# Kernel optimization log

Hardware: AMD Instinct MI355X
Metric: run time of the kernel (lower is better)

## Reference

```python
import jax, jax.numpy as jnp
import numpy as np

B, S = 16, 512
VOCAB = 32000
EMB = 512
HID = 1024
LAT = 256
NLAYERS = 2


def rnn_layer(x_seq, h0, w_ih, w_hh, b_ih, b_hh):
    # x_seq: [B, S, in_dim], h0: [B, H]; vanilla tanh RNN (nn.RNN semantics)
    # precompute input projection outside the scan
    xw = jnp.einsum('bsi,hi->bsh', x_seq, w_ih) + b_ih + b_hh  # [B, S, H]

    def step(h, xt):
        h_new = jnp.tanh(xt + h @ w_hh.T)
        return h_new, h_new

    _, ys = jax.lax.scan(step, h0, jnp.swapaxes(xw, 0, 1))  # scan over time
    return jnp.swapaxes(ys, 0, 1)  # [B, S, H]


def setup_inputs() -> dict:
    key = jax.random.key(0)
    ks = jax.random.split(key, 16)
    sc = 0.02
    inp = {
        'z': jax.random.normal(ks[0], (B, LAT), dtype=jnp.float32),
        'inp': jax.random.randint(ks[1], (B, S), 0, VOCAB),
        'emb_table': jax.random.normal(ks[2], (VOCAB, EMB), dtype=jnp.float32) * sc,
        'l2h_w': jax.random.normal(ks[3], (LAT, HID * NLAYERS), dtype=jnp.float32) * sc,
        'l2h_b': jnp.zeros((HID * NLAYERS,), dtype=jnp.float32),
        'w_ih0': jax.random.normal(ks[4], (HID, EMB), dtype=jnp.float32) * sc,
        'w_hh0': jax.random.normal(ks[5], (HID, HID), dtype=jnp.float32) * sc,
        'b_ih0': jnp.zeros((HID,), dtype=jnp.float32),
        'b_hh0': jnp.zeros((HID,), dtype=jnp.float32),
        'w_ih1': jax.random.normal(ks[6], (HID, HID), dtype=jnp.float32) * sc,
        'w_hh1': jax.random.normal(ks[7], (HID, HID), dtype=jnp.float32) * sc,
        'b_ih1': jnp.zeros((HID,), dtype=jnp.float32),
        'b_hh1': jnp.zeros((HID,), dtype=jnp.float32),
        'pred_w': jax.random.normal(ks[8], (HID, VOCAB), dtype=jnp.float32) * sc,
        'pred_b': jnp.zeros((VOCAB,), dtype=jnp.float32),
    }
    return inp


def reference(z, inp, emb_table, l2h_w, l2h_b, w_ih0, w_hh0, b_ih0, b_hh0,
              w_ih1, w_hh1, b_ih1, b_hh1, pred_w, pred_b):
    batch = z.shape[0]
    # latent2hidden, then view(hidden_factor, batch, H) as in torch (flat reshape)
    hidden = z @ l2h_w + l2h_b                      # [B, H*L]
    hidden = hidden.reshape(NLAYERS, batch, HID)     # [L, B, H]
    x = emb_table[inp]                               # [B, S, EMB]
    h1 = rnn_layer(x, hidden[0], w_ih0, w_hh0, b_ih0, b_hh0)   # [B, S, H]
    h2 = rnn_layer(h1, hidden[1], w_ih1, w_hh1, b_ih1, b_hh1)  # [B, S, H]
    logits = h2 @ pred_w + pred_b                    # [B, S, VOCAB]
    return logits
```

## Files before the change

kernel.cpp:

```cpp
#include <hip/hip_runtime.h>
#include <hip/hip_bf16.h>

#define BB 16
#define SS 512
#define VOCAB 32000
#define EMB 512
#define HID 1024
#define LAT 256

typedef __attribute__((ext_vector_type(8))) short bf16x8v;
typedef __attribute__((ext_vector_type(4))) float f32x4v;

__device__ __forceinline__ unsigned short f2b(float f) {
  unsigned int u = __float_as_uint(f);
  unsigned int r = (u + 0x7fffu + ((u >> 16) & 1u)) >> 16;
  return (unsigned short)r;
}

__device__ __forceinline__ float b2f(unsigned short s) {
  return __uint_as_float(((unsigned int)s) << 16);
}

__device__ __forceinline__ float fast_tanh(float x) {
  float t = fminf(fmaxf(x * 2.8853900817779268f, -60.f), 60.f);
  float e = __builtin_amdgcn_exp2f(t);
  return (e - 1.f) * __builtin_amdgcn_rcpf(e + 1.f);
}

__device__ __forceinline__ bf16x8v load16_coherent(const unsigned short* p) {
  bf16x8v r;
  asm volatile("global_load_dwordx4 %0, %1, off sc0 sc1"
               : "=v"(r) : "v"(p) : "memory");
  return r;
}

#define WAITV(n)                                                   \
  do {                                                             \
    asm volatile("s_waitcnt vmcnt(" #n ")" ::: "memory");          \
    __builtin_amdgcn_sched_barrier(0);                             \
  } while (0)

#define MCHUNK(HF, WROW, K0, A)                                              \
  _Pragma("unroll")                                                          \
  for (int kk = K0; kk < K0 + 8; ++kk) {                                     \
    bf16x8v bw = *(const bf16x8v*)&Ws[(WROW) * LDW + kk * 32 + fg * 8];      \
    A = __builtin_amdgcn_mfma_f32_16x16x32_bf16(HF[kk], bw, A, 0, 0, 0);     \
  }

__global__ __launch_bounds__(256) void k_f2b(const float* __restrict__ src,
                                             unsigned short* __restrict__ dst, int n) {
  int i = blockIdx.x * 256 + threadIdx.x;
  int stride = gridDim.x * 256;
  for (; i < n; i += stride) dst[i] = f2b(src[i]);
}

__global__ __launch_bounds__(256) void k_misc(const float* __restrict__ bih0, const float* __restrict__ bhh0,
                                              const float* __restrict__ bih1, const float* __restrict__ bhh1,
                                              float* __restrict__ bias0, float* __restrict__ bias1,
                                              unsigned int* __restrict__ flags, int nflags) {
  int i = blockIdx.x * 256 + threadIdx.x;
  if (i < HID) { bias0[i] = bih0[i] + bhh0[i]; bias1[i] = bih1[i] + bhh1[i]; }
  if (i < nflags) flags[i] = 0u;
}

__global__ __launch_bounds__(256) void k_latent(const float* __restrict__ z, const float* __restrict__ w,
                                                const float* __restrict__ bvec, unsigned short* __restrict__ h0) {
  int idx = blockIdx.x * 256 + threadIdx.x;
  int l  = idx >> 14;
  int bb = (idx >> 10) & 15;
  int hh = idx & 1023;
  int b = l * 8 + (bb >> 1);
  int j = ((bb & 1) << 10) | hh;
  float s = bvec[j];
  for (int k = 0; k < LAT; ++k) s += z[b * LAT + k] * w[k * (HID * 2) + j];
  h0[idx] = f2b(s);
}

__global__ __launch_bounds__(256) void k_embed(const float* __restrict__ emb, const int* __restrict__ inp,
                                               unsigned short* __restrict__ x) {
  int row = blockIdx.x;
  int tok = inp[row];
  for (int j = threadIdx.x; j < EMB; j += 256)
    x[(long)row * EMB + j] = f2b(emb[(long)tok * EMB + j]);
}

__global__ void k_transpose(const float* __restrict__ src, unsigned short* __restrict__ dst) {
  __shared__ float tile[32][33];
  int n0 = blockIdx.x * 32;
  int k0 = blockIdx.y * 32;
  int tx = threadIdx.x, ty = threadIdx.y;
  for (int i = ty; i < 32; i += 8)
    tile[i][tx] = src[(long)(k0 + i) * VOCAB + n0 + tx];
  __syncthreads();
  for (int i = ty; i < 32; i += 8)
    dst[(long)(n0 + i) * HID + k0 + tx] = f2b(tile[tx][i]);
}

template <typename OUT>
__global__ __launch_bounds__(256) void gemm_bt(const unsigned short* __restrict__ A,
                                               const unsigned short* __restrict__ Bm,
                                               const float* __restrict__ bias,
                                               OUT* __restrict__ C,
                                               int M, int N, int K) {
  const int LDT = 72;
  extern __shared__ unsigned short smem_g[];
  unsigned short* As = smem_g;
  unsigned short* Bs = smem_g + 128 * LDT;

  int nTn = N >> 7;
  int tm = blockIdx.x / nTn, tn = blockIdx.x % nTn;
  long m0 = (long)tm << 7, n0 = (long)tn << 7;
  int t = threadIdx.x;
  int lane = t & 63, w = t >> 6;
  int wr = (w >> 1) * 64, wc = (w & 1) * 64;
  int fr = lane & 15, fg = lane >> 4;

  f32x4v acc[4][4];
  f32x4v zero = {0.f, 0.f, 0.f, 0.f};
#pragma unroll
  for (int i = 0; i < 4; ++i)
#pragma unroll
    for (int j = 0; j < 4; ++j) acc[i][j] = zero;

  int srow = t >> 3;
  int scol = (t & 7) << 3;

  for (int kt = 0; kt < K; kt += 64) {
#pragma unroll
    for (int it = 0; it < 4; ++it) {
      int row = srow + it * 32;
      bf16x8v va = *(const bf16x8v*)&A[(m0 + row) * K + kt + scol];
      bf16x8v vb = *(const bf16x8v*)&Bm[(n0 + row) * K + kt + scol];
      *(bf16x8v*)&As[row * LDT + scol] = va;
      *(bf16x8v*)&Bs[row * LDT + scol] = vb;
    }
    __syncthreads();
#pragma unroll
    for (int kk = 0; kk < 2; ++kk) {
      int ko = kk * 32 + fg * 8;
      bf16x8v af[4], bfv[4];
#pragma unroll
      for (int i = 0; i < 4; ++i) af[i] = *(const bf16x8v*)&As[(wr + i * 16 + fr) * LDT + ko];
#pragma unroll
      for (int j = 0; j < 4; ++j) bfv[j] = *(const bf16x8v*)&Bs[(wc + j * 16 + fr) * LDT + ko];
#pragma unroll
      for (int i = 0; i < 4; ++i)
#pragma unroll
        for (int j = 0; j < 4; ++j)
          acc[i][j] = __builtin_amdgcn_mfma_f32_16x16x32_bf16(af[i], bfv[j], acc[i][j], 0, 0, 0);
    }
    __syncthreads();
  }

#pragma unroll
  for (int j = 0; j < 4; ++j) {
    long n = n0 + wc + j * 16 + fr;
    float bv = bias[n];
#pragma unroll
    for (int i = 0; i < 4; ++i) {
      long mrow = m0 + wr + i * 16 + fg * 4;
#pragma unroll
      for (int r = 0; r < 4; ++r) {
        float v = acc[i][j][r] + bv;
        if constexpr (__hip_internal::is_same<OUT, float>::value) {
          C[(mrow + r) * (long)N + n] = v;
        } else {
          C[(mrow + r) * (long)N + n] = f2b(v);
        }
      }
    }
  }
}

__global__ __launch_bounds__(128, 1) void k_scan2(const unsigned short* __restrict__ whh0,
                                                  const unsigned short* __restrict__ wih1,
                                                  const unsigned short* __restrict__ whh1,
                                                  const unsigned short* __restrict__ xw0,
                                                  const float* __restrict__ bias1,
                                                  const unsigned short* __restrict__ h0all,
                                                  unsigned short* __restrict__ ys0,
                                                  unsigned short* __restrict__ ys1,
                                                  unsigned int* __restrict__ flags) {
  const int LDW = 1032;
  extern __shared__ unsigned short Ws[];
  float* Part = (float*)(Ws + 32 * LDW);
  const int tid = threadIdx.x;
  const int lane = tid & 63;
  const int wv = tid >> 6;
  const int fr = lane & 15, fg = lane >> 4;
  const int wg = blockIdx.x;
  const f32x4v zero = {0.f, 0.f, 0.f, 0.f};

  if (wg < 32) {
    const int nbase = wg * 32;
    for (int c = tid; c < 32 * 128; c += 128) {
      int row = c >> 7, col = (c & 127) << 3;
      *(bf16x8v*)&Ws[row * LDW + col] = *(const bf16x8v*)&whh0[(long)(nbase + row) * HID + col];
    }
    __syncthreads();

    const int wrow = wv * 16 + fr;
    const int mycol = nbase + wrow;
    const int odd = fr & 1;

    for (int t = 0; t < SS; ++t) {
      unsigned short xv[4];
#pragma unroll
      for (int r = 0; r < 4; ++r)
        xv[r] = xw0[((long)(fg * 4 + r) * SS + t) * HID + mycol];

      if (t > 0) {
        unsigned tgt = (unsigned)t;
        for (;;) {
          unsigned v = 0xffffffffu;
          if (lane < 32)
            v = __hip_atomic_load(&flags[lane << 4], __ATOMIC_RELAXED, __HIP_MEMORY_SCOPE_AGENT);
          if (__all(v >= tgt)) break;
        }
      }
      const unsigned short* hp = (t == 0) ? (h0all + (long)fr * HID)
                                          : (ys0 + ((long)fr * SS + (t - 1)) * HID);
      bf16x8v hf[32];
#pragma unroll
      for (int kk = 0; kk < 32; ++kk) hf[kk] = load16_coherent(&hp[kk * 32 + fg * 8]);
      __builtin_amdgcn_sched_barrier(0);

      f32x4v aA = zero, aB = zero;
      WAITV(24); MCHUNK(hf, wrow, 0,  aA);
      WAITV(16); MCHUNK(hf, wrow, 8,  aB);
      WAITV(8);  MCHUNK(hf, wrow, 16, aA);
      WAITV(0);  MCHUNK(hf, wrow, 24, aB);
      f32x4v acc = aA + aB;

      unsigned av[4], pv[4];
#pragma unroll
      for (int r = 0; r < 4; ++r) {
        av[r] = (unsigned)f2b(fast_tanh(acc[r] + b2f(xv[r])));
        pv[r] = __shfl_xor(av[r], 1);
      }
      if (!odd) {
#pragma unroll
        for (int r = 0; r < 4; ++r)
          __hip_atomic_store((unsigned int*)&ys0[((long)(fg * 4 + r) * SS + t) * HID + mycol],
                             av[r] | (pv[r] << 16), __ATOMIC_RELAXED, __HIP_MEMORY_SCOPE_AGENT);
      }
      WAITV(0);
      __syncthreads();
      if (tid == 0)
        __hip_atomic_store(&flags[wg << 4], (unsigned)(t + 1),
                           __ATOMIC_RELAXED, __HIP_MEMORY_SCOPE_AGENT);
    }
  } else {
    const int j = wg - 32;
    const int nbase = j * 16;
    for (int c = tid; c < 32 * 128; c += 128) {
      int row = c >> 7, col = (c & 127) << 3;
      const unsigned short* src = (row < 16) ? &wih1[(long)(nbase + row) * HID + col]
                                             : &whh1[(long)(nbase + row - 16) * HID + col];
      *(bf16x8v*)&Ws[row * LDW + col] = *(const bf16x8v*)src;
    }
    __syncthreads();
    const int odd = fr & 1;

    if (wv == 0) {
      const float bv = bias1[nbase + fr];
      for (int t = 0; t < SS; ++t) {
        {
          unsigned tgt = (unsigned)(t + 1);
          for (;;) {
            unsigned v = 0xffffffffu;
            if (lane < 32)
              v = __hip_atomic_load(&flags[lane << 4], __ATOMIC_RELAXED, __HIP_MEMORY_SCOPE_AGENT);
            if (__all(v >= tgt)) break;
          }
        }
        const unsigned short* hp1 = ys0 + ((long)fr * SS + t) * HID;
        bf16x8v hf[32];
#pragma unroll
        for (int kk = 0; kk < 32; ++kk) hf[kk] = load16_coherent(&hp1[kk * 32 + fg * 8]);
        __builtin_amdgcn_sched_barrier(0);

        f32x4v aA = zero, aB = zero;
        WAITV(24); MCHUNK(hf, fr, 0,  aA);
        WAITV(16); MCHUNK(hf, fr, 8,  aB);
        WAITV(8);  MCHUNK(hf, fr, 16, aA);
        WAITV(0);  MCHUNK(hf, fr, 24, aB);

        __syncthreads();
        f32x4v part = *(const f32x4v*)&Part[lane << 2];
        f32x4v sum = (aA + aB) + part;

        unsigned av[4], pv[4];
#pragma unroll
        for (int r = 0; r < 4; ++r) {
          av[r] = (unsigned)f2b(fast_tanh(sum[r] + bv));
          pv[r] = __shfl_xor(av[r], 1);
        }
        if (!odd) {
#pragma unroll
          for (int r = 0; r < 4; ++r)
            __hip_atomic_store((unsigned int*)&ys1[((long)(fg * 4 + r) * SS + t) * HID + nbase + fr],
                               av[r] | (pv[r] << 16), __ATOMIC_RELAXED, __HIP_MEMORY_SCOPE_AGENT);
        }
        WAITV(0);
        if (lane == 0)
          __hip_atomic_store(&flags[1024 + (j << 4)], (unsigned)(t + 1),
                             __ATOMIC_RELAXED, __HIP_MEMORY_SCOPE_AGENT);
      }
    } else {
      for (int t = 0; t < SS; ++t) {
        if (t > 0) {
          unsigned tgt = (unsigned)t;
          for (;;) {
            unsigned v = __hip_atomic_load(&flags[1024 + (lane << 4)],
                                           __ATOMIC_RELAXED, __HIP_MEMORY_SCOPE_AGENT);
            if (__all(v >= tgt)) break;
          }
        }
        const unsigned short* hp2 = (t == 0) ? (h0all + (long)(BB + fr) * HID)
                                             : (ys1 + ((long)fr * SS + (t - 1)) * HID);
        bf16x8v hf[32];
#pragma unroll
        for (int kk = 0; kk < 32; ++kk) hf[kk] = load16_coherent(&hp2[kk * 32 + fg * 8]);
        __builtin_amdgcn_sched_barrier(0);

        f32x4v aA = zero, aB = zero;
        WAITV(24); MCHUNK(hf, 16 + fr, 0,  aA);
        WAITV(16); MCHUNK(hf, 16 + fr, 8,  aB);
        WAITV(8);  MCHUNK(hf, 16 + fr, 16, aA);
        WAITV(0);  MCHUNK(hf, 16 + fr, 24, aB);

        *(f32x4v*)&Part[lane << 2] = aA + aB;
        __syncthreads();
      }
    }
  }
}

extern "C" void kernel_launch(void* const* d_in, const int* in_sizes, int n_in,
                              void* d_out, int out_size, void* d_ws, size_t ws_size,
                              hipStream_t stream) {
  const float* z     = (const float*)d_in[0];
  const int*   inp   = (const int*)d_in[1];
  const float* emb   = (const float*)d_in[2];
  const float* l2h_w = (const float*)d_in[3];
  const float* l2h_b = (const float*)d_in[4];
  const float* wih0  = (const float*)d_in[5];
  const float* whh0  = (const float*)d_in[6];
  const float* bih0  = (const float*)d_in[7];
  const float* bhh0  = (const float*)d_in[8];
  const float* wih1  = (const float*)d_in[9];
  const float* whh1  = (const float*)d_in[10];
  const float* bih1  = (const float*)d_in[11];
  const float* bhh1  = (const float*)d_in[12];
  const float* predw = (const float*)d_in[13];
  const float* predb = (const float*)d_in[14];
  float* out = (float*)d_out;

  char* ws = (char*)d_ws;
  size_t off = 0;
  auto alloc = [&](size_t bytes) {
    char* p = ws + off;
    off = (off + bytes + 255) & ~(size_t)255;
    return p;
  };
  unsigned short* xb     = (unsigned short*)alloc((size_t)BB * SS * EMB * 2);
  unsigned short* wih0b  = (unsigned short*)alloc((size_t)HID * EMB * 2);
  unsigned short* whh0b  = (unsigned short*)alloc((size_t)HID * HID * 2);
  unsigned short* wih1b  = (unsigned short*)alloc((size_t)HID * HID * 2);
  unsigned short* whh1b  = (unsigned short*)alloc((size_t)HID * HID * 2);
  unsigned short* predTb = (unsigned short*)alloc((size_t)VOCAB * HID * 2);
  unsigned short* xw0    = (unsigned short*)alloc((size_t)BB * SS * HID * 2);
  unsigned short* ys0    = (unsigned short*)alloc((size_t)BB * SS * HID * 2);
  unsigned short* ys1    = (unsigned short*)alloc((size_t)BB * SS * HID * 2);
  unsigned short* h0b    = (unsigned short*)alloc((size_t)2 * BB * HID * 2);
  float*          bias0  = (float*)alloc((size_t)HID * 4);
  float*          bias1  = (float*)alloc((size_t)HID * 4);
  unsigned int*   flags  = (unsigned int*)alloc((size_t)2048 * 4);

  k_f2b<<<256, 256, 0, stream>>>(wih0, wih0b, HID * EMB);
  k_f2b<<<256, 256, 0, stream>>>(whh0, whh0b, HID * HID);
  k_f2b<<<256, 256, 0, stream>>>(wih1, wih1b, HID * HID);
  k_f2b<<<256, 256, 0, stream>>>(whh1, whh1b, HID * HID);
  k_misc<<<8, 256, 0, stream>>>(bih0, bhh0, bih1, bhh1, bias0, bias1, flags, 2048);
  k_latent<<<(2 * BB * HID) / 256, 256, 0, stream>>>(z, l2h_w, l2h_b, h0b);
  k_embed<<<BB * SS, 256, 0, stream>>>(emb, inp, xb);
  k_transpose<<<dim3(VOCAB / 32, HID / 32), dim3(32, 8), 0, stream>>>(predw, predTb);

  size_t gemm_lds = (size_t)2 * 128 * 72 * 2;
  size_t scan_lds = (size_t)32 * 1032 * 2 + 64 * 4 * 4;

  gemm_bt<unsigned short><<<(BB * SS / 128) * (HID / 128), 256, gemm_lds, stream>>>(
      xb, wih0b, bias0, xw0, BB * SS, HID, EMB);
  k_scan2<<<96, 128, scan_lds, stream>>>(whh0b, wih1b, whh1b, xw0, bias1, h0b, ys0, ys1, flags);
  gemm_bt<float><<<(BB * SS / 128) * (VOCAB / 128), 256, gemm_lds, stream>>>(
      ys1, predTb, predb, out, BB * SS, VOCAB, HID);
}
```

Baseline: 2.995 ms.

## Fuse vocab projection GEMM into scan kernel and overlap with recurrence

Switches embedding, xw0 and hidden-state buffers to time-major layout so each 128-row tile holds 8 complete time steps. It then launches 256 extra workgroups inside the scan kernel that poll the layer-1 flags and compute the vocab projection tile by tile as timesteps finish. This is meant to hide the large output GEMM behind the serial recurrence. The cost is that the fused GEMM is simple and unpipelined (no double buffering, 64-wide N tiles), its blocks compete with the scan blocks for CUs and memory bandwidth, and the design relies on all 352 blocks being co-resident.

After: 4.632 ms. 54.7% more time.

```diff
diff --git a/kernel.cpp b/kernel.cpp
--- a/kernel.cpp
+++ b/kernel.cpp
@@ -79,9 +79,11 @@
 __global__ __launch_bounds__(256) void k_embed(const float* __restrict__ emb, const int* __restrict__ inp,
                                                unsigned short* __restrict__ x) {
   int row = blockIdx.x;
+  int b = row >> 9, t = row & (SS - 1);
   int tok = inp[row];
+  long drow = (long)t * BB + b;
   for (int j = threadIdx.x; j < EMB; j += 256)
-    x[(long)row * EMB + j] = f2b(emb[(long)tok * EMB + j]);
+    x[drow * EMB + j] = f2b(emb[(long)tok * EMB + j]);
 }
 
 __global__ void k_transpose(const float* __restrict__ src, unsigned short* __restrict__ dst) {
@@ -180,7 +182,10 @@
                                                   const unsigned short* __restrict__ h0all,
                                                   unsigned short* __restrict__ ys0,
                                                   unsigned short* __restrict__ ys1,
-                                                  unsigned int* __restrict__ flags) {
+                                                  unsigned int* __restrict__ flags,
+                                                  const unsigned short* __restrict__ predTb,
+                                                  const float* __restrict__ predb,
+                                                  float* __restrict__ out) {
   const int LDW = 1032;
   extern __shared__ unsigned short Ws[];
   float* Part = (float*)(Ws + 32 * LDW);
@@ -207,7 +212,7 @@
       unsigned short xv[4];
 #pragma unroll
       for (int r = 0; r < 4; ++r)
-        xv[r] = xw0[((long)(fg * 4 + r) * SS + t) * HID + mycol];
+        xv[r] = xw0[((long)t * BB + fg * 4 + r) * HID + mycol];
 
       if (t > 0) {
         unsigned tgt = (unsigned)t;
@@ -219,7 +224,7 @@
         }
       }
       const unsigned short* hp = (t == 0) ? (h0all + (long)fr * HID)
-                                          : (ys0 + ((long)fr * SS + (t - 1)) * HID);
+                                          : (ys0 + ((long)(t - 1) * BB + fr) * HID);
       bf16x8v hf[32];
 #pragma unroll
       for (int kk = 0; kk < 32; ++kk) hf[kk] = load16_coherent(&hp[kk * 32 + fg * 8]);
@@ -241,7 +246,7 @@
       if (!odd) {
 #pragma unroll
         for (int r = 0; r < 4; ++r)
-          __hip_atomic_store((unsigned int*)&ys0[((long)(fg * 4 + r) * SS + t) * HID + mycol],
+          __hip_atomic_store((unsigned int*)&ys0[((long)t * BB + fg * 4 + r) * HID + mycol],
                              av[r] | (pv[r] << 16), __ATOMIC_RELAXED, __HIP_MEMORY_SCOPE_AGENT);
       }
       WAITV(0);
@@ -250,7 +255,7 @@
         __hip_atomic_store(&flags[wg << 4], (unsigned)(t + 1),
                            __ATOMIC_RELAXED, __HIP_MEMORY_SCOPE_AGENT);
     }
-  } else {
+  } else if (wg < 96) {
     const int j = wg - 32;
     const int nbase = j * 16;
     for (int c = tid; c < 32 * 128; c += 128) {
@@ -274,7 +279,7 @@
             if (__all(v >= tgt)) break;
           }
         }
-        const unsigned short* hp1 = ys0 + ((long)fr * SS + t) * HID;
+        const unsigned short* hp1 = ys0 + ((long)t * BB + fr) * HID;
         bf16x8v hf[32];
 #pragma unroll
         for (int kk = 0; kk < 32; ++kk) hf[kk] = load16_coherent(&hp1[kk * 32 + fg * 8]);
@@ -299,7 +304,7 @@
         if (!odd) {
 #pragma unroll
           for (int r = 0; r < 4; ++r)
-            __hip_atomic_store((unsigned int*)&ys1[((long)(fg * 4 + r) * SS + t) * HID + nbase + fr],
+            __hip_atomic_store((unsigned int*)&ys1[((long)t * BB + fg * 4 + r) * HID + nbase + fr],
                                av[r] | (pv[r] << 16), __ATOMIC_RELAXED, __HIP_MEMORY_SCOPE_AGENT);
         }
         WAITV(0);
@@ -318,7 +323,7 @@
           }
         }
         const unsigned short* hp2 = (t == 0) ? (h0all + (long)(BB + fr) * HID)
-                                             : (ys1 + ((long)fr * SS + (t - 1)) * HID);
+                                             : (ys1 + ((long)(t - 1) * BB + fr) * HID);
         bf16x8v hf[32];
 #pragma unroll
         for (int kk = 0; kk < 32; ++kk) hf[kk] = load16_coherent(&hp2[kk * 32 + fg * 8]);
@@ -332,6 +337,79 @@
 
         *(f32x4v*)&Part[lane << 2] = aA + aB;
         __syncthreads();
+      }
+    }
+  } else {
+    const int wid = wg - 96;
+    unsigned short* As = Ws;
+    unsigned short* Bs = Ws + 128 * 72;
+    const int NT = VOCAB / 64;
+    const int brow = tid >> 1;
+    const int bcol = (tid & 1) * 32;
+
+    for (int tau = wid; tau < 64 * NT; tau += 256) {
+      int mt = tau / NT, nt = tau - mt * NT;
+      long m0 = (long)mt << 7, n0 = (long)nt << 6;
+
+      unsigned need = (unsigned)(mt * 8 + 8);
+      for (;;) {
+        unsigned v = 0xffffffffu;
+        v = __hip_atomic_load(&flags[1024 + (lane << 4)], __ATOMIC_RELAXED, __HIP_MEMORY_SCOPE_AGENT);
+        if (__all(v >= need)) break;
+        __builtin_amdgcn_s_sleep(32);
+      }
+
+      f32x4v acc[4][4];
+#pragma unroll
+      for (int i = 0; i < 4; ++i)
+#pragma unroll
+        for (int jj = 0; jj < 4; ++jj) acc[i][jj] = zero;
+
+      for (int kt = 0; kt < HID; kt += 64) {
+        bf16x8v avv[8];
+#pragma unroll
+        for (int c = 0; c < 8; ++c)
+          avv[c] = load16_coherent(&ys1[(m0 + tid) * HID + kt + c * 8]);
+        bf16x8v bvv[4];
+        const unsigned short* bp = &predTb[(n0 + brow) * HID + kt + bcol];
+#pragma unroll
+        for (int c = 0; c < 4; ++c) bvv[c] = *(const bf16x8v*)&bp[c * 8];
+        WAITV(0);
+        __syncthreads();
+#pragma unroll
+        for (int c = 0; c < 8; ++c) *(bf16x8v*)&As[tid * 72 + c * 8] = avv[c];
+#pragma unroll
+        for (int c = 0; c < 4; ++c) *(bf16x8v*)&Bs[brow * 72 + bcol + c * 8] = bvv[c];
+        __syncthreads();
+#pragma unroll
+        for (int kk = 0; kk < 2; ++kk) {
+          int ko = kk * 32 + fg * 8;
+          bf16x8v af[4], bf2[4];
+#pragma unroll
+          for (int i = 0; i < 4; ++i) af[i] = *(const bf16x8v*)&As[(wv * 64 + i * 16 + fr) * 72 + ko];
+#pragma unroll
+          for (int jj = 0; jj < 4; ++jj) bf2[jj] = *(const bf16x8v*)&Bs[(jj * 16 + fr) * 72 + ko];
+#pragma unroll
+          for (int i = 0; i < 4; ++i)
+#pragma unroll
+            for (int jj = 0; jj < 4; ++jj)
+              acc[i][jj] = __builtin_amdgcn_mfma_f32_16x16x32_bf16(af[i], bf2[jj], acc[i][jj], 0, 0, 0);
+        }
+      }
+
+#pragma unroll
+      for (int jj = 0; jj < 4; ++jj) {
+        long col = n0 + jj * 16 + fr;
+        float bz = predb[col];
+#pragma unroll
+        for (int i = 0; i < 4; ++i) {
+#pragma unroll
+          for (int r = 0; r < 4; ++r) {
+            long mrow = m0 + wv * 64 + i * 16 + fg * 4 + r;
+            long t = mrow >> 4, b = mrow & 15;
+            out[(b * SS + t) * VOCAB + col] = acc[i][jj][r] + bz;
+          }
+        }
       }
     }
   }
@@ -392,7 +470,6 @@
 
   gemm_bt<unsigned short><<<(BB * SS / 128) * (HID / 128), 256, gemm_lds, stream>>>(
       xb, wih0b, bias0, xw0, BB * SS, HID, EMB);
-  k_scan2<<<96, 128, scan_lds, stream>>>(whh0b, wih1b, whh1b, xw0, bias1, h0b, ys0, ys1, flags);
-  gemm_bt<float><<<(BB * SS / 128) * (VOCAB / 128), 256, gemm_lds, stream>>>(
-      ys1, predTb, predb, out, BB * SS, VOCAB, HID);
-}
+  k_scan2<<<352, 128, scan_lds, stream>>>(whh0b, wih1b, whh1b, xw0, bias1, h0b, ys0, ys1,
+                                          flags, predTb, predb, out);
+}
```

## Replace flag-based inter-block sync with NaN-sentinel data polling in RNN scan

Applied to the files above, without the earlier changes.

Removes the per-step flag counters and barriers. The hidden-state buffers are pre-filled with a NaN bf16 sentinel, and consumers repeatedly load the previous hidden vector and run the MFMA reduction until no NaN appears. This drops one flag round-trip and the block barrier from every recurrent step. In exchange, it adds two full-buffer sentinel fill kernels and may redo matmuls while data is still partial. It also relies on genuine NaNs never occurring and on atomic 64-bit loads being coherent.

After: 5.000 ms. +67.0%, slower.

```diff
diff --git a/kernel.cpp b/kernel.cpp
--- a/kernel.cpp
+++ b/kernel.cpp
@@ -7,9 +7,13 @@
 #define EMB 512
 #define HID 1024
 #define LAT 256
+#define SENT 0x7FC07FC0u
 
 typedef __attribute__((ext_vector_type(8))) short bf16x8v;
 typedef __attribute__((ext_vector_type(4))) float f32x4v;
+typedef __attribute__((ext_vector_type(4))) unsigned int u32x4v;
+typedef __attribute__((ext_vector_type(2))) unsigned long long u64x2v;
+typedef unsigned long long u64;
 
 __device__ __forceinline__ unsigned short f2b(float f) {
   unsigned int u = __float_as_uint(f);
@@ -27,24 +31,32 @@
   return (e - 1.f) * __builtin_amdgcn_rcpf(e + 1.f);
 }
 
-__device__ __forceinline__ bf16x8v load16_coherent(const unsigned short* p) {
-  bf16x8v r;
-  asm volatile("global_load_dwordx4 %0, %1, off sc0 sc1"
-               : "=v"(r) : "v"(p) : "memory");
-  return r;
-}
-
-#define WAITV(n)                                                   \
-  do {                                                             \
-    asm volatile("s_waitcnt vmcnt(" #n ")" ::: "memory");          \
-    __builtin_amdgcn_sched_barrier(0);                             \
-  } while (0)
-
-#define MCHUNK(HF, WROW, K0, A)                                              \
-  _Pragma("unroll")                                                          \
-  for (int kk = K0; kk < K0 + 8; ++kk) {                                     \
-    bf16x8v bw = *(const bf16x8v*)&Ws[(WROW) * LDW + kk * 32 + fg * 8];      \
-    A = __builtin_amdgcn_mfma_f32_16x16x32_bf16(HF[kk], bw, A, 0, 0, 0);     \
+__device__ __forceinline__ u64 aload64(const u64* p) {
+  return __hip_atomic_load(p, __ATOMIC_RELAXED, __HIP_MEMORY_SCOPE_AGENT);
+}
+
+#define VALID_MM(P64, WROW, AA, AB)                                           \
+  for (;;) {                                                                  \
+    u64 hu[64];                                                               \
+    _Pragma("unroll")                                                         \
+    for (int kk = 0; kk < 32; ++kk) {                                         \
+      hu[2 * kk]     = aload64(&(P64)[kk * 8 + fg * 2]);                      \
+      hu[2 * kk + 1] = aload64(&(P64)[kk * 8 + fg * 2 + 1]);                  \
+    }                                                                         \
+    AA = zero; AB = zero;                                                     \
+    _Pragma("unroll")                                                         \
+    for (int kk = 0; kk < 32; ++kk) {                                         \
+      u64x2v tq; tq[0] = hu[2 * kk]; tq[1] = hu[2 * kk + 1];                  \
+      bf16x8v hf = __builtin_bit_cast(bf16x8v, tq);                           \
+      bf16x8v bw = *(const bf16x8v*)&Ws[(WROW) * LDW + kk * 32 + fg * 8];     \
+      if (kk & 1) AB = __builtin_amdgcn_mfma_f32_16x16x32_bf16(hf, bw, AB, 0, 0, 0); \
+      else        AA = __builtin_amdgcn_mfma_f32_16x16x32_bf16(hf, bw, AA, 0, 0, 0); \
+    }                                                                         \
+    int bad = 0;                                                              \
+    _Pragma("unroll")                                                         \
+    for (int r = 0; r < 4; ++r)                                               \
+      bad |= __builtin_isnan(AA[r]) | __builtin_isnan(AB[r]);                 \
+    if (!__any(bad)) break;                                                   \
   }
 
 __global__ __launch_bounds__(256) void k_f2b(const float* __restrict__ src,
@@ -54,13 +66,18 @@
   for (; i < n; i += stride) dst[i] = f2b(src[i]);
 }
 
+__global__ __launch_bounds__(256) void k_sentinel(unsigned int* __restrict__ p, long n4) {
+  long i = (long)blockIdx.x * 256 + threadIdx.x;
+  long stride = (long)gridDim.x * 256;
+  u32x4v s = {SENT, SENT, SENT, SENT};
+  for (; i < n4; i += stride) ((u32x4v*)p)[i] = s;
+}
+
 __global__ __launch_bounds__(256) void k_misc(const float* __restrict__ bih0, const float* __restrict__ bhh0,
                                               const float* __restrict__ bih1, const float* __restrict__ bhh1,
-                                              float* __restrict__ bias0, float* __restrict__ bias1,
-                                              unsigned int* __restrict__ flags, int nflags) {
+                                              float* __restrict__ bias0, float* __restrict__ bias1) {
   int i = blockIdx.x * 256 + threadIdx.x;
   if (i < HID) { bias0[i] = bih0[i] + bhh0[i]; bias1[i] = bih1[i] + bhh1[i]; }
-  if (i < nflags) flags[i] = 0u;
 }
 
 __global__ __launch_bounds__(256) void k_latent(const float* __restrict__ z, const float* __restrict__ w,
@@ -179,8 +196,7 @@
                                                   const float* __restrict__ bias1,
                                                   const unsigned short* __restrict__ h0all,
                                                   unsigned short* __restrict__ ys0,
-                                                  unsigned short* __restrict__ ys1,
-                                                  unsigned int* __restrict__ flags) {
+                                                  unsigned short* __restrict__ ys1) {
   const int LDW = 1032;
   extern __shared__ unsigned short Ws[];
   float* Part = (float*)(Ws + 32 * LDW);
@@ -209,27 +225,10 @@
       for (int r = 0; r < 4; ++r)
         xv[r] = xw0[((long)(fg * 4 + r) * SS + t) * HID + mycol];
 
-      if (t > 0) {
-        unsigned tgt = (unsigned)t;
-        for (;;) {
-          unsigned v = 0xffffffffu;
-          if (lane < 32)
-            v = __hip_atomic_load(&flags[lane << 4], __ATOMIC_RELAXED, __HIP_MEMORY_SCOPE_AGENT);
-          if (__all(v >= tgt)) break;
-        }
-      }
-      const unsigned short* hp = (t == 0) ? (h0all + (long)fr * HID)
-                                          : (ys0 + ((long)fr * SS + (t - 1)) * HID);
-      bf16x8v hf[32];
-#pragma unroll
-      for (int kk = 0; kk < 32; ++kk) hf[kk] = load16_coherent(&hp[kk * 32 + fg * 8]);
-      __builtin_amdgcn_sched_barrier(0);
-
-      f32x4v aA = zero, aB = zero;
-      WAITV(24); MCHUNK(hf, wrow, 0,  aA);
-      WAITV(16); MCHUNK(hf, wrow, 8,  aB);
-      WAITV(8);  MCHUNK(hf, wrow, 16, aA);
-      WAITV(0);  MCHUNK(hf, wrow, 24, aB);
+      const u64* p64 = (const u64*)((t == 0) ? (h0all + (long)fr * HID)
+                                             : (ys0 + ((long)fr * SS + (t - 1)) * HID));
+      f32x4v aA, aB;
+      VALID_MM(p64, wrow, aA, aB);
       f32x4v acc = aA + aB;
 
       unsigned av[4], pv[4];
@@ -244,11 +243,6 @@
           __hip_atomic_store((unsigned int*)&ys0[((long)(fg * 4 + r) * SS + t) * HID + mycol],
                              av[r] | (pv[r] << 16), __ATOMIC_RELAXED, __HIP_MEMORY_SCOPE_AGENT);
       }
-      WAITV(0);
-      __syncthreads();
-      if (tid == 0)
-        __hip_atomic_store(&flags[wg << 4], (unsigned)(t + 1),
-                           __ATOMIC_RELAXED, __HIP_MEMORY_SCOPE_AGENT);
     }
   } else {
     const int j = wg - 32;
@@ -265,26 +259,9 @@
     if (wv == 0) {
       const float bv = bias1[nbase + fr];
       for (int t = 0; t < SS; ++t) {
-        {
-          unsigned tgt = (unsigned)(t + 1);
-          for (;;) {
-            unsigned v = 0xffffffffu;
-            if (lane < 32)
-              v = __hip_atomic_load(&flags[lane << 4], __ATOMIC_RELAXED, __HIP_MEMORY_SCOPE_AGENT);
-            if (__all(v >= tgt)) break;
-          }
-        }
-        const unsigned short* hp1 = ys0 + ((long)fr * SS + t) * HID;
-        bf16x8v hf[32];
-#pragma unroll
-        for (int kk = 0; kk < 32; ++kk) hf[kk] = load16_coherent(&hp1[kk * 32 + fg * 8]);
-        __builtin_amdgcn_sched_barrier(0);
-
-        f32x4v aA = zero, aB = zero;
-        WAITV(24); MCHUNK(hf, fr, 0,  aA);
-        WAITV(16); MCHUNK(hf, fr, 8,  aB);
-        WAITV(8);  MCHUNK(hf, fr, 16, aA);
-        WAITV(0);  MCHUNK(hf, fr, 24, aB);
+        const u64* p64 = (const u64*)(ys0 + ((long)fr * SS + t) * HID);
+        f32x4v aA, aB;
+        VALID_MM(p64, fr, aA, aB);
 
         __syncthreads();
         f32x4v part = *(const f32x4v*)&Part[lane << 2];
@@ -302,33 +279,13 @@
             __hip_atomic_store((unsigned int*)&ys1[((long)(fg * 4 + r) * SS + t) * HID + nbase + fr],
                                av[r] | (pv[r] << 16), __ATOMIC_RELAXED, __HIP_MEMORY_SCOPE_AGENT);
         }
-        WAITV(0);
-        if (lane == 0)
-          __hip_atomic_store(&flags[1024 + (j << 4)], (unsigned)(t + 1),
-                             __ATOMIC_RELAXED, __HIP_MEMORY_SCOPE_AGENT);
       }
     } else {
       for (int t = 0; t < SS; ++t) {
-        if (t > 0) {
-          unsigned tgt = (unsigned)t;
-          for (;;) {
-            unsigned v = __hip_atomic_load(&flags[1024 + (lane << 4)],
-                                           __ATOMIC_RELAXED, __HIP_MEMORY_SCOPE_AGENT);
-            if (__all(v >= tgt)) break;
-          }
-        }
-        const unsigned short* hp2 = (t == 0) ? (h0all + (long)(BB + fr) * HID)
-                                             : (ys1 + ((long)fr * SS + (t - 1)) * HID);
-        bf16x8v hf[32];
-#pragma unroll
-        for (int kk = 0; kk < 32; ++kk) hf[kk] = load16_coherent(&hp2[kk * 32 + fg * 8]);
-        __builtin_amdgcn_sched_barrier(0);
-
-        f32x4v aA = zero, aB = zero;
-        WAITV(24); MCHUNK(hf, 16 + fr, 0,  aA);
-        WAITV(16); MCHUNK(hf, 16 + fr, 8,  aB);
-        WAITV(8);  MCHUNK(hf, 16 + fr, 16, aA);
-        WAITV(0);  MCHUNK(hf, 16 + fr, 24, aB);
+        const u64* p64 = (const u64*)((t == 0) ? (h0all + (long)(BB + fr) * HID)
+                                               : (ys1 + ((long)fr * SS + (t - 1)) * HID));
+        f32x4v aA, aB;
+        VALID_MM(p64, 16 + fr, aA, aB);
 
         *(f32x4v*)&Part[lane << 2] = aA + aB;
         __syncthreads();
@@ -376,23 +333,24 @@
   unsigned short* h0b    = (unsigned short*)alloc((size_t)2 * BB * HID * 2);
   float*          bias0  = (float*)alloc((size_t)HID * 4);
   float*          bias1  = (float*)alloc((size_t)HID * 4);
-  unsigned int*   flags  = (unsigned int*)alloc((size_t)2048 * 4);
 
   k_f2b<<<256, 256, 0, stream>>>(wih0, wih0b, HID * EMB);
   k_f2b<<<256, 256, 0, stream>>>(whh0, whh0b, HID * HID);
   k_f2b<<<256, 256, 0, stream>>>(wih1, wih1b, HID * HID);
   k_f2b<<<256, 256, 0, stream>>>(whh1, whh1b, HID * HID);
-  k_misc<<<8, 256, 0, stream>>>(bih0, bhh0, bih1, bhh1, bias0, bias1, flags, 2048);
+  k_misc<<<4, 256, 0, stream>>>(bih0, bhh0, bih1, bhh1, bias0, bias1);
   k_latent<<<(2 * BB * HID) / 256, 256, 0, stream>>>(z, l2h_w, l2h_b, h0b);
   k_embed<<<BB * SS, 256, 0, stream>>>(emb, inp, xb);
   k_transpose<<<dim3(VOCAB / 32, HID / 32), dim3(32, 8), 0, stream>>>(predw, predTb);
+  k_sentinel<<<2048, 256, 0, stream>>>((unsigned int*)ys0, (long)BB * SS * HID / 8);
+  k_sentinel<<<2048, 256, 0, stream>>>((unsigned int*)ys1, (long)BB * SS * HID / 8);
 
   size_t gemm_lds = (size_t)2 * 128 * 72 * 2;
   size_t scan_lds = (size_t)32 * 1032 * 2 + 64 * 4 * 4;
 
   gemm_bt<unsigned short><<<(BB * SS / 128) * (HID / 128), 256, gemm_lds, stream>>>(
       xb, wih0b, bias0, xw0, BB * SS, HID, EMB);
-  k_scan2<<<96, 128, scan_lds, stream>>>(whh0b, wih1b, whh1b, xw0, bias1, h0b, ys0, ys1, flags);
+  k_scan2<<<96, 128, scan_lds, stream>>>(whh0b, wih1b, whh1b, xw0, bias1, h0b, ys0, ys1);
   gemm_bt<float><<<(BB * SS / 128) * (VOCAB / 128), 256, gemm_lds, stream>>>(
       ys1, predTb, predb, out, BB * SS, VOCAB, HID);
 }
```
